# Kernel optimization log

Measured on AMD Instinct MI355X. Metric: run time of the kernel, lower is better.

The kernel has to match this reference:

```python
import jax, jax.numpy as jnp
import numpy as np
import math

N_NODES = 100000
N_EDGES = 600000
HIDDEN = 128
HEADS = 8
HEAD_DIM = HIDDEN // HEADS
TEMPORAL = 32


def _xavier(key, fan_in, fan_out):
    bound = math.sqrt(6.0 / (fan_in + fan_out))
    return jax.random.uniform(key, (fan_in, fan_out), jnp.float32, -bound, bound)


def setup_inputs() -> dict:
    key = jax.random.key(0)
    ks = jax.random.split(key, 16)
    inp = {
        'query': jax.random.normal(ks[0], (N_NODES, HIDDEN), jnp.float32),
        'key': jax.random.normal(ks[1], (N_NODES, HIDDEN), jnp.float32),
        'value': jax.random.normal(ks[2], (N_NODES, HIDDEN), jnp.float32),
        'temporal_encoding': jax.random.normal(ks[3], (N_EDGES, TEMPORAL), jnp.float32),
        'edge_index': jax.random.randint(ks[4], (2, N_EDGES), 0, N_NODES, jnp.int64),
        # projection weights stored as [in, out] so y = x @ W + b
        'Wq': _xavier(ks[5], HIDDEN, HIDDEN), 'bq': jnp.zeros((HIDDEN,), jnp.float32),
        'Wk': _xavier(ks[6], HIDDEN, HIDDEN), 'bk': jnp.zeros((HIDDEN,), jnp.float32),
        'Wv': _xavier(ks[7], HIDDEN, HIDDEN), 'bv': jnp.zeros((HIDDEN,), jnp.float32),
        'Wtq': _xavier(ks[8], TEMPORAL, HIDDEN), 'btq': jnp.zeros((HIDDEN,), jnp.float32),
        'Wtk': _xavier(ks[9], TEMPORAL, HIDDEN), 'btk': jnp.zeros((HIDDEN,), jnp.float32),
        'Wout': _xavier(ks[10], HIDDEN, HIDDEN), 'bout': jnp.zeros((HIDDEN,), jnp.float32),
    }
    return inp


def reference(query, key, value, temporal_encoding, edge_index,
              Wq, bq, Wk, bk, Wv, bv, Wtq, btq, Wtk, btk, Wout, bout):
    n = query.shape[0]
    H, hd = HEADS, HEAD_DIM
    Q = (query @ Wq + bq).reshape(n, H, hd)
    K = (key @ Wk + bk).reshape(n, H, hd)
    V = (value @ Wv + bv).reshape(n, H, hd)
    tq = (temporal_encoding @ Wtq + btq).reshape(-1, H, hd)
    tk = (temporal_encoding @ Wtk + btk).reshape(-1, H, hd)

    src, tgt = edge_index[0], edge_index[1]
    # per-edge, per-head scores [E, H]
    scores = jnp.sum(Q[src] * K[tgt], axis=-1) / math.sqrt(hd)
    scores = scores + jnp.sum(tq * tk, axis=-1)

    # segment softmax over edges grouped by target node (stable, per head)
    seg_max = jax.ops.segment_max(scores, tgt, num_segments=n)  # [N, H]
    e = jnp.exp(scores - seg_max[tgt])
    seg_sum = jax.ops.segment_sum(e, tgt, num_segments=n)       # [N, H]
    attn_weights = e / seg_sum[tgt]                              # [E, H]

    # weighted scatter-add aggregation of source values onto targets
    agg = jax.ops.segment_sum(attn_weights[..., None] * V[src], tgt, num_segments=n)  # [N, H, hd]
    attn_output = agg.reshape(n, HIDDEN) @ Wout + bout
    return attn_output, attn_weights
```

## Files before the change

### kernel.cpp

```cpp
#include <hip/hip_runtime.h>
#include <hip/hip_bf16.h>

#define HID 128
#define MAXD 64
#define TBLK 512

typedef __attribute__((ext_vector_type(8))) short bfrag8;
typedef __attribute__((ext_vector_type(4))) short bf4;
typedef __attribute__((ext_vector_type(4))) float facc4;

__device__ inline short f2bf(float x) {
  unsigned u = __builtin_bit_cast(unsigned, x);
  u += 0x7fffu + ((u >> 16) & 1u);
  return (short)(u >> 16);
}
__device__ inline float bf2f(short s) {
  unsigned u = ((unsigned)(unsigned short)s) << 16;
  return __builtin_bit_cast(float, u);
}

__global__ __launch_bounds__(256) void init_k(
    const float* __restrict__ Wq, const float* __restrict__ Wk,
    const float* __restrict__ Wv, const float* __restrict__ Wout,
    const float* __restrict__ Wtq, const float* __restrict__ Wtk,
    short* __restrict__ out, int* __restrict__ degcur, int n2) {
  int gid = blockIdx.x * 256 + threadIdx.x;
  if (gid < n2) degcur[gid] = 0;
  if (gid >= 9216) return;
  bfrag8 v;
  if (gid < 8192) {
    int which = gid >> 11;
    int chunk = gid & 2047;
    const float* W = (which == 0) ? Wq : (which == 1) ? Wk
                   : (which == 2) ? Wv : Wout;
    int c  = chunk & 15;
    int g  = (chunk >> 4) & 3;
    int kt = (chunk >> 6) & 3;
    int ct = chunk >> 8;
    int col = ct * 16 + c;
    int k0 = kt * 32 + g * 8;
    #pragma unroll
    for (int i = 0; i < 8; ++i) v[i] = f2bf(W[(size_t)(k0 + i) * HID + col]);
  } else {
    int chunk = gid - 8192;
    int c  = chunk & 15;
    int g  = (chunk >> 4) & 3;
    int ct = (chunk >> 6) & 7;
    int qk = chunk >> 9;
    const float* W = qk ? Wtk : Wtq;
    int col = ct * 16 + c;
    int k0 = g * 8;
    #pragma unroll
    for (int i = 0; i < 8; ++i) v[i] = f2bf(W[(size_t)(k0 + i) * HID + col]);
  }
  *(bfrag8*)(out + (size_t)gid * 8) = v;
}

template <typename IT, typename OT, int MODE>
__device__ __forceinline__ void gemm_body(
    short* __restrict__ Ws, float* __restrict__ bshf, const IT* __restrict__ X,
    const short* __restrict__ Wp, const float* __restrict__ b,
    OT* __restrict__ Y, int nrows, int ch) {
  const int t = threadIdx.x;
  #pragma unroll
  for (int it = 0; it < 4; ++it) {
    int chunk = t + it * 512;
    *(bfrag8*)(&Ws[chunk * 8]) = *(const bfrag8*)(Wp + (size_t)chunk * 8);
  }
  if (t < 128) bshf[t] = b[t];
  __syncthreads();

  const int w  = t >> 6;
  const int l  = t & 63;
  const int lr = l & 15;
  const int g  = l >> 4;

  const int row0 = ch * 128 + w * 16;
  const int arow = min(row0 + lr, nrows - 1);

  facc4 acc[8];
  #pragma unroll
  for (int ct = 0; ct < 8; ++ct)
    acc[ct] = *(const facc4*)(&bshf[ct * 16 + g * 4]);

  #pragma unroll
  for (int kt = 0; kt < 4; ++kt) {
    bfrag8 a;
    if constexpr (sizeof(IT) == 4) {
      const float* xp = (const float*)X + (size_t)arow * HID + kt * 32 + g * 8;
      float xv[8];
      *(facc4*)(xv)     = *(const facc4*)(xp);
      *(facc4*)(xv + 4) = *(const facc4*)(xp + 4);
      #pragma unroll
      for (int i = 0; i < 8; ++i) a[i] = f2bf(xv[i]);
    } else {
      a = *(const bfrag8*)((const short*)X + (size_t)arow * HID + kt * 32 + g * 8);
    }
    #pragma unroll
    for (int ct = 0; ct < 8; ++ct) {
      bfrag8 bf = *(const bfrag8*)(&Ws[(((ct * 4 + kt) * 4 + g) * 16 + lr) * 8]);
      acc[ct] = __builtin_amdgcn_mfma_f32_16x16x32_bf16(bf, a, acc[ct], 0, 0, 0);
    }
  }

  const int row = row0 + lr;
  if (row < nrows) {
    #pragma unroll
    for (int ct = 0; ct < 8; ++ct) {
      const int col0 = ct * 16 + g * 4;
      if constexpr (sizeof(OT) == 4) {
        *(facc4*)((float*)Y + (size_t)row * HID + col0) = acc[ct];
      } else {
        bf4 p;
        #pragma unroll
        for (int j = 0; j < 4; ++j) p[j] = f2bf(acc[ct][j]);
        size_t base;
        if constexpr (MODE == 0) base = (size_t)row * HID + col0;
        else base = (size_t)row * 256 + col0 + (MODE == 2 ? 128 : 0);
        *(bf4*)((short*)Y + base) = p;
      }
    }
  }
}

__device__ __forceinline__ void temporal_body(
    short* __restrict__ Ws, float* __restrict__ bsh, float* __restrict__ tsh,
    const float* __restrict__ T, const short* __restrict__ Wp,
    const float* __restrict__ btq, const float* __restrict__ btk,
    float* __restrict__ ts, int E, int ntiles, int bx, int nblk) {
  const int t = threadIdx.x;
  #pragma unroll
  for (int it = 0; it < 2; ++it) {
    int chunk = t + it * 512;
    *(bfrag8*)(&Ws[chunk * 8]) = *(const bfrag8*)(Wp + (size_t)chunk * 8);
  }
  if (t < 256) bsh[t] = (t < 128) ? btq[t] : btk[t - 128];
  __syncthreads();

  const int w = t >> 6;
  const int l = t & 63;
  const int c = l & 15;
  const int g = l >> 4;
  float* mytsh = tsh + w * 160;

  for (int tile = bx; tile < ntiles; tile += nblk) {
    const int e0 = tile * 128 + w * 16;
    const int ar = min(e0 + c, E - 1);
    const float* tp = T + (size_t)ar * 32 + g * 8;
    float xv[8];
    *(facc4*)(xv)     = *(const facc4*)(tp);
    *(facc4*)(xv + 4) = *(const facc4*)(tp + 4);
    bfrag8 tb;
    #pragma unroll
    for (int i = 0; i < 8; ++i) tb[i] = f2bf(xv[i]);

    #pragma unroll 1
    for (int ct = 0; ct < 8; ++ct) {
      facc4 accq = *(const facc4*)(&bsh[ct * 16 + g * 4]);
      bfrag8 wq = *(const bfrag8*)(&Ws[(ct * 64 + g * 16 + c) * 8]);
      accq = __builtin_amdgcn_mfma_f32_16x16x32_bf16(wq, tb, accq, 0, 0, 0);
      facc4 acck = *(const facc4*)(&bsh[128 + ct * 16 + g * 4]);
      bfrag8 wk = *(const bfrag8*)(&Ws[(512 + ct * 64 + g * 16 + c) * 8]);
      acck = __builtin_amdgcn_mfma_f32_16x16x32_bf16(wk, tb, acck, 0, 0, 0);

      float s = accq[0] * acck[0] + accq[1] * acck[1] +
                accq[2] * acck[2] + accq[3] * acck[3];
      s += __shfl_xor(s, 16, 64);
      s += __shfl_xor(s, 32, 64);
      if (g == 0) mytsh[c * 10 + ct] = s;
    }
    int e = e0 + (l >> 2);
    if (e < E) {
      float2 v2 = *(const float2*)(&mytsh[(l >> 2) * 10 + (l & 3) * 2]);
      *(float2*)(ts + (size_t)e0 * 8 + l * 2) = v2;
    }
  }
}

__global__ __launch_bounds__(512, 6) void mega_k(
    const float* __restrict__ query, const float* __restrict__ key,
    const float* __restrict__ value, const float* __restrict__ temporal,
    const short* __restrict__ Wpre,
    const float* __restrict__ bq, const float* __restrict__ bk,
    const float* __restrict__ bv, const float* __restrict__ btq,
    const float* __restrict__ btk,
    short* __restrict__ QVp, short* __restrict__ Kp,
    float* __restrict__ tscores, const int* __restrict__ tgt,
    int* __restrict__ deg, int N, int E, int nch, int ntiles) {
  __shared__ __align__(16) char smem[33280];
  short* Ws = (short*)smem;
  float* baux = (float*)(smem + 32768);
  const int bx = blockIdx.x;
  if (bx < 3 * nch) {
    const int role = bx % 3;
    const int ch = bx / 3;
    if (role == 0)
      gemm_body<float, short, 1>(Ws, baux, query, Wpre + 0 * 16384, bq, QVp, N, ch);
    else if (role == 1)
      gemm_body<float, short, 0>(Ws, baux, key, Wpre + 1 * 16384, bk, Kp, N, ch);
    else
      gemm_body<float, short, 2>(Ws, baux, value, Wpre + 2 * 16384, bv, QVp, N, ch);
  } else if (bx < 3 * nch + TBLK) {
    temporal_body(Ws, (float*)(smem + 16384), (float*)(smem + 17408),
                  temporal, Wpre + 4 * 16384, btq, btk, tscores, E, ntiles,
                  bx - 3 * nch, TBLK);
  } else {
    int gid = (bx - 3 * nch - TBLK) * 512 + threadIdx.x;
    if (gid < E) atomicAdd(&deg[tgt[gid]], 1);
  }
}

template <typename IT, typename OT, int MODE>
__global__ __launch_bounds__(512, 6) void gemm_mfma_k(
    const IT* __restrict__ X, const short* __restrict__ Wp,
    const float* __restrict__ b, OT* __restrict__ Y, int nrows) {
  __shared__ __align__(16) char smem[33280];
  gemm_body<IT, OT, MODE>((short*)smem, (float*)(smem + 32768), X, Wp, b, Y,
                          nrows, blockIdx.x);
}

__global__ __launch_bounds__(256) void block_sum_k(const int* __restrict__ deg,
                                                   int* __restrict__ bsum, int n) {
  __shared__ int sd[256];
  const int base = blockIdx.x * 1024;
  const int t = threadIdx.x;
  int s = 0;
  #pragma unroll
  for (int j = 0; j < 4; ++j) {
    int i = base + t + j * 256;
    if (i < n) s += deg[i];
  }
  sd[t] = s;
  __syncthreads();
  for (int st = 128; st; st >>= 1) {
    if (t < st) sd[t] += sd[t + st];
    __syncthreads();
  }
  if (t == 0) bsum[blockIdx.x] = sd[0];
}

__global__ __launch_bounds__(1024) void scan_partials_k(const int* __restrict__ bsum,
                                                        int* __restrict__ boff, int G) {
  __shared__ int sd[1024];
  const int t = threadIdx.x;
  int v = (t < G) ? bsum[t] : 0;
  sd[t] = v;
  __syncthreads();
  for (int s = 1; s < 1024; s <<= 1) {
    int a = (t >= s) ? sd[t - s] : 0;
    __syncthreads();
    sd[t] += a;
    __syncthreads();
  }
  if (t < G) boff[t] = sd[t] - v;
}

__global__ __launch_bounds__(256) void block_scan_k(const int* __restrict__ deg,
                                                    const int* __restrict__ boff,
                                                    int* __restrict__ off, int n) {
  __shared__ int sd[256];
  const int base = blockIdx.x * 1024;
  const int t = threadIdx.x;
  const int i0 = base + t * 4;
  int v[4];
  int s = 0;
  #pragma unroll
  for (int j = 0; j < 4; ++j) {
    v[j] = (i0 + j < n) ? deg[i0 + j] : 0;
    s += v[j];
  }
  const int own = s;
  sd[t] = s;
  __syncthreads();
  for (int st = 1; st < 256; st <<= 1) {
    int a = (t >= st) ? sd[t - st] : 0;
    __syncthreads();
    sd[t] += a;
    __syncthreads();
  }
  int acc = boff[blockIdx.x] + sd[t] - own;
  #pragma unroll
  for (int j = 0; j < 4; ++j) {
    int idx = i0 + j;
    if (idx < n) {
      off[idx] = acc;
      acc += v[j];
      if (idx == n - 1) off[n] = acc;
    }
  }
}

__global__ __launch_bounds__(256) void scatter_k(const int* __restrict__ src,
                                                 const int* __restrict__ tgt,
                                                 const int* __restrict__ off,
                                                 int* __restrict__ cur,
                                                 int2* __restrict__ elist2, int E) {
  int gid = blockIdx.x * 256 + threadIdx.x;
  if (gid < E) {
    int n = tgt[gid];
    int p = atomicAdd(&cur[n], 1);
    elist2[off[n] + p] = make_int2(gid, src[gid]);
  }
}

__global__ __launch_bounds__(256) void softmax_agg_k(
    const float* __restrict__ tscores, const short* __restrict__ QVp,
    const short* __restrict__ Kp, const int* __restrict__ off,
    const int2* __restrict__ elist2, float* __restrict__ attn_w,
    short* __restrict__ aggb, int N) {
  __shared__ int esh[8][MAXD];
  __shared__ int ssh[8][MAXD];
  __shared__ float sraw[8][MAXD][8];
  const int t = threadIdx.x;
  const int grp = t >> 5;
  const int g = t & 31;
  const int h = g >> 2;
  const int j = g & 3;
  const int n = blockIdx.x * 8 + grp;
  if (n >= N) return;

  const int s0 = off[n];
  const int deg = off[n + 1] - s0;

  float kr[4];
  {
    bf4 k4 = *(const bf4*)(Kp + (size_t)n * HID + g * 4);
    #pragma unroll
    for (int q = 0; q < 4; ++q) kr[q] = bf2f(k4[q]);
  }

  if (deg <= MAXD) {
    for (int i = g; i < deg; i += 32) {
      int2 es = elist2[s0 + i];
      esh[grp][i] = es.x;
      ssh[grp][i] = es.y;
    }

    float lsum = 0.f;
    float a0 = 0.f, a1 = 0.f, a2 = 0.f, a3 = 0.f;
    int i = 0;
    for (; i + 4 <= deg; i += 4) {
      const size_t b0 = (size_t)ssh[grp][i]     * 256 + g * 4;
      const size_t b1 = (size_t)ssh[grp][i + 1] * 256 + g * 4;
      const size_t b2 = (size_t)ssh[grp][i + 2] * 256 + g * 4;
      const size_t b3 = (size_t)ssh[grp][i + 3] * 256 + g * 4;
      bf4 q0 = *(const bf4*)(QVp + b0);
      bf4 q1 = *(const bf4*)(QVp + b1);
      bf4 q2 = *(const bf4*)(QVp + b2);
      bf4 q3 = *(const bf4*)(QVp + b3);
      bf4 v0 = *(const bf4*)(QVp + b0 + 128);
      bf4 v1 = *(const bf4*)(QVp + b1 + 128);
      bf4 v2 = *(const bf4*)(QVp + b2 + 128);
      bf4 v3 = *(const bf4*)(QVp + b3 + 128);
      float ts0 = tscores[(size_t)esh[grp][i]     * 8 + h];
      float ts1 = tscores[(size_t)esh[grp][i + 1] * 8 + h];
      float ts2 = tscores[(size_t)esh[grp][i + 2] * 8 + h];
      float ts3 = tscores[(size_t)esh[grp][i + 3] * 8 + h];
      float p0 = bf2f(q0[0]) * kr[0] + bf2f(q0[1]) * kr[1] +
                 bf2f(q0[2]) * kr[2] + bf2f(q0[3]) * kr[3];
      float p1 = bf2f(q1[0]) * kr[0] + bf2f(q1[1]) * kr[1] +
                 bf2f(q1[2]) * kr[2] + bf2f(q1[3]) * kr[3];
      float p2 = bf2f(q2[0]) * kr[0] + bf2f(q2[1]) * kr[1] +
                 bf2f(q2[2]) * kr[2] + bf2f(q2[3]) * kr[3];
      float p3 = bf2f(q3[0]) * kr[0] + bf2f(q3[1]) * kr[1] +
                 bf2f(q3[2]) * kr[2] + bf2f(q3[3]) * kr[3];
      p0 += __shfl_xor(p0, 1, 4); p0 += __shfl_xor(p0, 2, 4);
      p1 += __shfl_xor(p1, 1, 4); p1 += __shfl_xor(p1, 2, 4);
      p2 += __shfl_xor(p2, 1, 4); p2 += __shfl_xor(p2, 2, 4);
      p3 += __shfl_xor(p3, 1, 4); p3 += __shfl_xor(p3, 2, 4);
      float w0 = __expf(ts0 + p0 * 0.25f);
      float w1 = __expf(ts1 + p1 * 0.25f);
      float w2 = __expf(ts2 + p2 * 0.25f);
      float w3 = __expf(ts3 + p3 * 0.25f);
      if (j == 0) {
        sraw[grp][i][h]     = w0;
        sraw[grp][i + 1][h] = w1;
        sraw[grp][i + 2][h] = w2;
        sraw[grp][i + 3][h] = w3;
      }
      lsum += (w0 + w1) + (w2 + w3);
      a0 += w0 * bf2f(v0[0]) + w1 * bf2f(v1[0]) +
            w2 * bf2f(v2[0]) + w3 * bf2f(v3[0]);
      a1 += w0 * bf2f(v0[1]) + w1 * bf2f(v1[1]) +
            w2 * bf2f(v2[1]) + w3 * bf2f(v3[1]);
      a2 += w0 * bf2f(v0[2]) + w1 * bf2f(v1[2]) +
            w2 * bf2f(v2[2]) + w3 * bf2f(v3[2]);
      a3 += w0 * bf2f(v0[3]) + w1 * bf2f(v1[3]) +
            w2 * bf2f(v2[3]) + w3 * bf2f(v3[3]);
    }
    for (; i < deg; ++i) {
      const size_t b0 = (size_t)ssh[grp][i] * 256 + g * 4;
      bf4 q0 = *(const bf4*)(QVp + b0);
      bf4 v0 = *(const bf4*)(QVp + b0 + 128);
      float ts0 = tscores[(size_t)esh[grp][i] * 8 + h];
      float p0 = bf2f(q0[0]) * kr[0] + bf2f(q0[1]) * kr[1] +
                 bf2f(q0[2]) * kr[2] + bf2f(q0[3]) * kr[3];
      p0 += __shfl_xor(p0, 1, 4); p0 += __shfl_xor(p0, 2, 4);
      float w0 = __expf(ts0 + p0 * 0.25f);
      if (j == 0) sraw[grp][i][h] = w0;
      lsum += w0;
      a0 += w0 * bf2f(v0[0]);
      a1 += w0 * bf2f(v0[1]);
      a2 += w0 * bf2f(v0[2]);
      a3 += w0 * bf2f(v0[3]);
    }
    float invl = (lsum > 0.f) ? 1.0f / lsum : 0.f;

    bf4 st;
    st[0] = f2bf(a0 * invl); st[1] = f2bf(a1 * invl);
    st[2] = f2bf(a2 * invl); st[3] = f2bf(a3 * invl);
    *(bf4*)(aggb + (size_t)n * HID + g * 4) = st;

    if (j == 0) {
      for (int q = 0; q < deg; ++q)
        attn_w[(size_t)esh[grp][q] * 8 + h] = sraw[grp][q][h] * invl;
    }
  } else {
    float m = -3.0e38f;
    for (int q = 0; q < deg; ++q) {
      int2 es = elist2[s0 + q];
      bf4 q4 = *(const bf4*)(QVp + (size_t)es.y * 256 + g * 4);
      float p = bf2f(q4[0]) * kr[0] + bf2f(q4[1]) * kr[1] +
                bf2f(q4[2]) * kr[2] + bf2f(q4[3]) * kr[3];
      p += __shfl_xor(p, 1, 4); p += __shfl_xor(p, 2, 4);
      m = fmaxf(m, tscores[(size_t)es.x * 8 + h] + p * 0.25f);
    }
    float l = 0.f;
    for (int q = 0; q < deg; ++q) {
      int2 es = elist2[s0 + q];
      bf4 q4 = *(const bf4*)(QVp + (size_t)es.y * 256 + g * 4);
      float p = bf2f(q4[0]) * kr[0] + bf2f(q4[1]) * kr[1] +
                bf2f(q4[2]) * kr[2] + bf2f(q4[3]) * kr[3];
      p += __shfl_xor(p, 1, 4); p += __shfl_xor(p, 2, 4);
      l += __expf(tscores[(size_t)es.x * 8 + h] + p * 0.25f - m);
    }
    float invl = (l > 0.f) ? 1.0f / l : 0.f;
    float a0 = 0.f, a1 = 0.f, a2 = 0.f, a3 = 0.f;
    for (int q = 0; q < deg; ++q) {
      int2 es = elist2[s0 + q];
      bf4 q4 = *(const bf4*)(QVp + (size_t)es.y * 256 + g * 4);
      bf4 v4 = *(const bf4*)(QVp + (size_t)es.y * 256 + 128 + g * 4);
      float p = bf2f(q4[0]) * kr[0] + bf2f(q4[1]) * kr[1] +
                bf2f(q4[2]) * kr[2] + bf2f(q4[3]) * kr[3];
      p += __shfl_xor(p, 1, 4); p += __shfl_xor(p, 2, 4);
      float w = __expf(tscores[(size_t)es.x * 8 + h] + p * 0.25f - m) * invl;
      a0 += w * bf2f(v4[0]);
      a1 += w * bf2f(v4[1]);
      a2 += w * bf2f(v4[2]);
      a3 += w * bf2f(v4[3]);
      if (j == 0) attn_w[(size_t)es.x * 8 + h] = w;
    }
    bf4 st;
    st[0] = f2bf(a0); st[1] = f2bf(a1); st[2] = f2bf(a2); st[3] = f2bf(a3);
    *(bf4*)(aggb + (size_t)n * HID + g * 4) = st;
  }
}

extern "C" void kernel_launch(void* const* d_in, const int* in_sizes, int n_in,
                              void* d_out, int out_size, void* d_ws, size_t ws_size,
                              hipStream_t stream) {
  const float* query    = (const float*)d_in[0];
  const float* key      = (const float*)d_in[1];
  const float* value    = (const float*)d_in[2];
  const float* temporal = (const float*)d_in[3];
  const int*   eidx     = (const int*)d_in[4];
  const float* Wq   = (const float*)d_in[5];
  const float* bq   = (const float*)d_in[6];
  const float* Wk   = (const float*)d_in[7];
  const float* bk   = (const float*)d_in[8];
  const float* Wv   = (const float*)d_in[9];
  const float* bv   = (const float*)d_in[10];
  const float* Wtq  = (const float*)d_in[11];
  const float* btq  = (const float*)d_in[12];
  const float* Wtk  = (const float*)d_in[13];
  const float* btk  = (const float*)d_in[14];
  const float* Wout = (const float*)d_in[15];
  const float* bout = (const float*)d_in[16];

  const int N = in_sizes[0] / HID;
  const int E = in_sizes[4] / 2;
  const int* src = eidx;
  const int* tgt = eidx + E;

  char* ws = (char*)d_ws;
  short* QVp = (short*)ws;                     ws += (size_t)N * 256 * 2;
  short* Kp = (short*)ws;                      ws += (size_t)N * HID * 2;
  short* aggb = (short*)ws;                    ws += (size_t)N * HID * 2;
  float* tscores = (float*)ws;                 ws += (size_t)E * 8 * 4;
  int* deg   = (int*)ws;                       ws += (size_t)N * 4;
  int* cur   = (int*)ws;                       ws += (size_t)N * 4;
  int* off   = (int*)ws;                       ws += (size_t)(N + 2) * 4;
  int2* elist2 = (int2*)ws;                    ws += (size_t)E * 8;
  int* bsum  = (int*)ws;                       ws += 1024 * 4;
  int* boff  = (int*)ws;                       ws += 1024 * 4;
  short* Wpre = (short*)ws;

  const int G = (N + 1023) / 1024;
  const int nch = (N + 127) / 128;
  const int ntiles = (E + 127) / 128;
  const int cblk = (E + 511) / 512;

  dim3 b256(256), b512(512);
  init_k<<<(2 * N + 255) / 256, b256, 0, stream>>>(Wq, Wk, Wv, Wout, Wtq, Wtk,
                                                   Wpre, deg, 2 * N);
  mega_k<<<3 * nch + TBLK + cblk, b512, 0, stream>>>(
      query, key, value, temporal, Wpre, bq, bk, bv, btq, btk,
      QVp, Kp, tscores, tgt, deg, N, E, nch, ntiles);

  block_sum_k<<<G, b256, 0, stream>>>(deg, bsum, N);
  scan_partials_k<<<1, 1024, 0, stream>>>(bsum, boff, G);
  block_scan_k<<<G, b256, 0, stream>>>(deg, boff, off, N);
  scatter_k<<<(E + 255) / 256, b256, 0, stream>>>(src, tgt, off, cur, elist2, E);

  float* attn_w = (float*)d_out + (size_t)N * HID;
  softmax_agg_k<<<(N + 7) / 8, b256, 0, stream>>>(tscores, QVp, Kp, off,
                                                  elist2, attn_w, aggb, N);

  gemm_mfma_k<short, float, 0><<<nch, b512, 0, stream>>>(aggb, Wpre + 3 * 16384,
                                                         bout, (float*)d_out, N);
}
```

Baseline: 225.5 us.

## Stage GEMM and temporal inputs through LDS with 64-row tiles split across waves

The QKV projection GEMM now loads each 64-row input tile cooperatively into swizzled LDS as bf16, and each of the 8 waves computes 16 rows by 4 column tiles instead of 16 rows by 8. This halves the rows per block, doubling the GEMM block count and cutting per-wave accumulators and MFMAs. The temporal projection likewise stages its edge tile in LDS with coalesced loads before the MFMA fragments are read. LDS per block grows to about 49KB, which may reduce occupancy, and extra barriers are added inside the temporal tile loop.

Result: no change. 223.1 us (-1.1%).

```diff
diff --git a/kernel.cpp b/kernel.cpp
--- a/kernel.cpp
+++ b/kernel.cpp
@@ -58,9 +58,9 @@
 
 template <typename IT, typename OT, int MODE>
 __device__ __forceinline__ void gemm_body(
-    short* __restrict__ Ws, float* __restrict__ bshf, const IT* __restrict__ X,
-    const short* __restrict__ Wp, const float* __restrict__ b,
-    OT* __restrict__ Y, int nrows, int ch) {
+    short* __restrict__ Ws, float* __restrict__ bshf, short* __restrict__ Xs,
+    const IT* __restrict__ X, const short* __restrict__ Wp,
+    const float* __restrict__ b, OT* __restrict__ Y, int nrows, int ch) {
   const int t = threadIdx.x;
   #pragma unroll
   for (int it = 0; it < 4; ++it) {
@@ -68,52 +68,65 @@
     *(bfrag8*)(&Ws[chunk * 8]) = *(const bfrag8*)(Wp + (size_t)chunk * 8);
   }
   if (t < 128) bshf[t] = b[t];
+  if constexpr (sizeof(IT) == 4) {
+    int row = t >> 3;
+    int arow = min(ch * 64 + row, nrows - 1);
+    const float* xp = (const float*)X + (size_t)arow * HID + (t & 7) * 16;
+    float xv[16];
+    *(facc4*)(xv)      = *(const facc4*)(xp);
+    *(facc4*)(xv + 4)  = *(const facc4*)(xp + 4);
+    *(facc4*)(xv + 8)  = *(const facc4*)(xp + 8);
+    *(facc4*)(xv + 12) = *(const facc4*)(xp + 12);
+    bfrag8 p0, p1;
+    #pragma unroll
+    for (int i = 0; i < 8; ++i) { p0[i] = f2bf(xv[i]); p1[i] = f2bf(xv[8 + i]); }
+    int u0 = (t & 7) * 2;
+    *(bfrag8*)(&Xs[row * 128 + ((u0    ) ^ (row & 7)) * 8]) = p0;
+    *(bfrag8*)(&Xs[row * 128 + ((u0 + 1) ^ (row & 7)) * 8]) = p1;
+  }
   __syncthreads();
 
   const int w  = t >> 6;
   const int l  = t & 63;
   const int lr = l & 15;
   const int g  = l >> 4;
-
-  const int row0 = ch * 128 + w * 16;
-  const int arow = min(row0 + lr, nrows - 1);
-
-  facc4 acc[8];
-  #pragma unroll
-  for (int ct = 0; ct < 8; ++ct)
-    acc[ct] = *(const facc4*)(&bshf[ct * 16 + g * 4]);
+  const int ctbase = (w >> 2) * 4;
+  const int row0 = ch * 64 + (w & 3) * 16;
+  const int xr = (w & 3) * 16 + lr;
+
+  facc4 acc[4];
+  #pragma unroll
+  for (int c2 = 0; c2 < 4; ++c2)
+    acc[c2] = *(const facc4*)(&bshf[(ctbase + c2) * 16 + g * 4]);
 
   #pragma unroll
   for (int kt = 0; kt < 4; ++kt) {
     bfrag8 a;
     if constexpr (sizeof(IT) == 4) {
-      const float* xp = (const float*)X + (size_t)arow * HID + kt * 32 + g * 8;
-      float xv[8];
-      *(facc4*)(xv)     = *(const facc4*)(xp);
-      *(facc4*)(xv + 4) = *(const facc4*)(xp + 4);
-      #pragma unroll
-      for (int i = 0; i < 8; ++i) a[i] = f2bf(xv[i]);
+      a = *(const bfrag8*)(&Xs[xr * 128 + ((kt * 4 + g) ^ (xr & 7)) * 8]);
     } else {
+      int arow = min(row0 + lr, nrows - 1);
       a = *(const bfrag8*)((const short*)X + (size_t)arow * HID + kt * 32 + g * 8);
     }
     #pragma unroll
-    for (int ct = 0; ct < 8; ++ct) {
+    for (int c2 = 0; c2 < 4; ++c2) {
+      int ct = ctbase + c2;
       bfrag8 bf = *(const bfrag8*)(&Ws[(((ct * 4 + kt) * 4 + g) * 16 + lr) * 8]);
-      acc[ct] = __builtin_amdgcn_mfma_f32_16x16x32_bf16(bf, a, acc[ct], 0, 0, 0);
+      acc[c2] = __builtin_amdgcn_mfma_f32_16x16x32_bf16(bf, a, acc[c2], 0, 0, 0);
     }
   }
 
   const int row = row0 + lr;
   if (row < nrows) {
     #pragma unroll
-    for (int ct = 0; ct < 8; ++ct) {
-      const int col0 = ct * 16 + g * 4;
+    for (int c2 = 0; c2 < 4; ++c2) {
+      const int col0 = (ctbase + c2) * 16 + g * 4;
       if constexpr (sizeof(OT) == 4) {
-        *(facc4*)((float*)Y + (size_t)row * HID + col0) = acc[ct];
+        *(facc4*)((float*)Y + (size_t)row * HID + col0) = acc[c2];
       } else {
         bf4 p;
         #pragma unroll
-        for (int j = 0; j < 4; ++j) p[j] = f2bf(acc[ct][j]);
+        for (int j = 0; j < 4; ++j) p[j] = f2bf(acc[c2][j]);
         size_t base;
         if constexpr (MODE == 0) base = (size_t)row * HID + col0;
         else base = (size_t)row * 256 + col0 + (MODE == 2 ? 128 : 0);
@@ -125,9 +138,10 @@
 
 __device__ __forceinline__ void temporal_body(
     short* __restrict__ Ws, float* __restrict__ bsh, float* __restrict__ tsh,
-    const float* __restrict__ T, const short* __restrict__ Wp,
-    const float* __restrict__ btq, const float* __restrict__ btk,
-    float* __restrict__ ts, int E, int ntiles, int bx, int nblk) {
+    short* __restrict__ Ts, const float* __restrict__ T,
+    const short* __restrict__ Wp, const float* __restrict__ btq,
+    const float* __restrict__ btk, float* __restrict__ ts,
+    int E, int ntiles, int bx, int nblk) {
   const int t = threadIdx.x;
   #pragma unroll
   for (int it = 0; it < 2; ++it) {
@@ -144,15 +158,23 @@
   float* mytsh = tsh + w * 160;
 
   for (int tile = bx; tile < ntiles; tile += nblk) {
+    __syncthreads();
+    {
+      int r = t >> 2;
+      int ar = min(tile * 128 + r, E - 1);
+      const float* tp = T + (size_t)ar * 32 + (t & 3) * 8;
+      float xv[8];
+      *(facc4*)(xv)     = *(const facc4*)(tp);
+      *(facc4*)(xv + 4) = *(const facc4*)(tp + 4);
+      bfrag8 p;
+      #pragma unroll
+      for (int i = 0; i < 8; ++i) p[i] = f2bf(xv[i]);
+      *(bfrag8*)(&Ts[r * 40 + (t & 3) * 8]) = p;
+    }
+    __syncthreads();
+
     const int e0 = tile * 128 + w * 16;
-    const int ar = min(e0 + c, E - 1);
-    const float* tp = T + (size_t)ar * 32 + g * 8;
-    float xv[8];
-    *(facc4*)(xv)     = *(const facc4*)(tp);
-    *(facc4*)(xv + 4) = *(const facc4*)(tp + 4);
-    bfrag8 tb;
-    #pragma unroll
-    for (int i = 0; i < 8; ++i) tb[i] = f2bf(xv[i]);
+    bfrag8 tb = *(const bfrag8*)(&Ts[(w * 16 + c) * 40 + g * 8]);
 
     #pragma unroll 1
     for (int ct = 0; ct < 8; ++ct) {
@@ -187,21 +209,23 @@
     short* __restrict__ QVp, short* __restrict__ Kp,
     float* __restrict__ tscores, const int* __restrict__ tgt,
     int* __restrict__ deg, int N, int E, int nch, int ntiles) {
-  __shared__ __align__(16) char smem[33280];
+  __shared__ __align__(16) char smem[49664];
   short* Ws = (short*)smem;
-  float* baux = (float*)(smem + 32768);
   const int bx = blockIdx.x;
   if (bx < 3 * nch) {
+    float* baux = (float*)(smem + 32768);
+    short* Xs = (short*)(smem + 33280);
     const int role = bx % 3;
     const int ch = bx / 3;
     if (role == 0)
-      gemm_body<float, short, 1>(Ws, baux, query, Wpre + 0 * 16384, bq, QVp, N, ch);
+      gemm_body<float, short, 1>(Ws, baux, Xs, query, Wpre + 0 * 16384, bq, QVp, N, ch);
     else if (role == 1)
-      gemm_body<float, short, 0>(Ws, baux, key, Wpre + 1 * 16384, bk, Kp, N, ch);
+      gemm_body<float, short, 0>(Ws, baux, Xs, key, Wpre + 1 * 16384, bk, Kp, N, ch);
     else
-      gemm_body<float, short, 2>(Ws, baux, value, Wpre + 2 * 16384, bv, QVp, N, ch);
+      gemm_body<float, short, 2>(Ws, baux, Xs, value, Wpre + 2 * 16384, bv, QVp, N, ch);
   } else if (bx < 3 * nch + TBLK) {
     temporal_body(Ws, (float*)(smem + 16384), (float*)(smem + 17408),
+                  (short*)(smem + 23808),
                   temporal, Wpre + 4 * 16384, btq, btk, tscores, E, ntiles,
                   bx - 3 * nch, TBLK);
   } else {
@@ -214,9 +238,10 @@
 __global__ __launch_bounds__(512, 6) void gemm_mfma_k(
     const IT* __restrict__ X, const short* __restrict__ Wp,
     const float* __restrict__ b, OT* __restrict__ Y, int nrows) {
-  __shared__ __align__(16) char smem[33280];
-  gemm_body<IT, OT, MODE>((short*)smem, (float*)(smem + 32768), X, Wp, b, Y,
-                          nrows, blockIdx.x);
+  __shared__ __align__(16) char smem[49664];
+  gemm_body<IT, OT, MODE>((short*)smem, (float*)(smem + 32768),
+                          (short*)(smem + 33280), X, Wp, b, Y, nrows,
+                          blockIdx.x);
 }
 
 __global__ __launch_bounds__(256) void block_sum_k(const int* __restrict__ deg,
@@ -496,7 +521,7 @@
   short* Wpre = (short*)ws;
 
   const int G = (N + 1023) / 1024;
-  const int nch = (N + 127) / 128;
+  const int nch = (N + 63) / 64;
   const int ntiles = (E + 127) / 128;
   const int cblk = (E + 511) / 512;
 
```
